# Performance work log

Measured on AMD Instinct MI355X. Metric: run time of the kernel, lower is better.

The kernel has to match this reference:

```python
import jax, jax.numpy as jnp
import numpy as np

N_POINTS = 2_000_000
N_BATCH = 8


def cart2polar(xyz):
    rho = jnp.sqrt(xyz[:, 0] ** 2 + xyz[:, 1] ** 2)
    phi = jnp.arctan2(xyz[:, 1], xyz[:, 0])
    return jnp.stack((rho, phi, xyz[:, 2]), axis=1)


def setup_inputs() -> dict:
    key = jax.random.key(0)
    k1, k2, k3, k4 = jax.random.split(key, 4)
    xy = jax.random.uniform(k1, (N_POINTS, 2), minval=-50.0, maxval=50.0)
    z = jax.random.uniform(k2, (N_POINTS, 1), minval=-4.0, maxval=2.0)
    inten = jax.random.uniform(k3, (N_POINTS, 1))
    points = jnp.concatenate([xy, z, inten], axis=1)  # [N, 4]
    batch_idx = jnp.sort(jax.random.randint(k4, (N_POINTS,), 0, N_BATCH)).astype(jnp.int32)
    coors_range_xyz = jnp.array([[0.0, 50.0], [-np.pi, np.pi], [-4.0, 2.0]], dtype=jnp.float32)
    spatial_shape = np.array([480, 360, 32])  # static
    scale_list = np.array([2, 4, 1])          # module appends 1; static
    return dict(points=points, batch_idx=batch_idx,
                coors_range_xyz=coors_range_xyz,
                spatial_shape=spatial_shape, scale_list=scale_list)


def _unique_rows(bxyz, dims):
    # Encode [b, gx, gy, gz] rows into a single int32 key (max 8*480*360*32 ~ 44M).
    key = ((bxyz[:, 0] * dims[0] + bxyz[:, 1]) * dims[1] + bxyz[:, 2]) * dims[2] + bxyz[:, 3]
    order = jnp.argsort(key)
    sk = key[order]
    flags = jnp.concatenate([jnp.ones((1,), bool), sk[1:] != sk[:-1]])
    rank = jnp.cumsum(flags.astype(jnp.int32)) - 1          # unique-id per sorted row
    inv = jnp.zeros_like(rank).at[order].set(rank)           # inverse map, like torch.unique
    # first occurrence of each unique row (all rows with same rank are identical)
    unq = jnp.zeros_like(bxyz).at[rank].set(bxyz[order])     # padded to [N, 4]
    num_unique = rank[-1] + 1
    return unq, inv, num_unique


def reference(points, batch_idx, coors_range_xyz, spatial_shape, scale_list):
    pc = points[:, :3]
    xyz_pol = cart2polar(pc)
    lo = coors_range_xyz[:, 0]
    hi = coors_range_xyz[:, 1]
    crop = hi - lo
    ss_np = np.asarray(spatial_shape)
    outs = []
    for scale in [int(s) for s in np.asarray(scale_list)]:
        cells = jnp.asarray(np.ceil(ss_np / scale) - 1.0, dtype=xyz_pol.dtype)
        grid = jnp.floor((jnp.clip(xyz_pol, lo, hi) - lo) / crop * cells).astype(jnp.int32)
        bxyz = jnp.concatenate([batch_idx[:, None].astype(jnp.int32), grid], axis=1)  # [N,4]
        dims = np.ceil(ss_np / scale).astype(np.int64)
        unq, inv, num = _unique_rows(bxyz, dims)
        # reorder unique coords as [b, z, y, x], cast int32 (torch: unq[:, [0,3,2,1]])
        coors = jnp.concatenate([unq[:, 0:1], unq[:, 3:4], unq[:, 2:3], unq[:, 1:2]], axis=1).astype(jnp.int32)
        outs.extend([bxyz, inv, coors, num])
    return tuple(outs)
```

## Files before the change

### kernel.cpp

```cpp
#include <hip/hip_runtime.h>
#include <cstdint>

#define DI __device__ __forceinline__

constexpr int NPTS       = 2000000;
constexpr int STRIDE_OUT = 18000001;
constexpr int OFF_INV    = 8000000;
constexpr int OFF_COORS  = 10000000;
constexpr int OFF_NUM    = 18000000;

constexpr int R2W  = 172800;
constexpr int R4W  = 21600;
constexpr int R1W  = 1382400;
constexpr int RW0  = 0;
constexpr int RW1  = R2W;
constexpr int RW2  = R2W + R4W;
constexpr int WTOT = R2W + R4W + R1W;
constexpr int NB1  = (WTOT + 1023) / 1024;
constexpr int J2   = 8;
constexpr int P1   = 6;
constexpr int J1   = 4;
constexpr int S1W  = 28800;
constexpr int S1BITS = S1W * 32;

constexpr int NBLK_INV   = (NPTS + 255) / 256;
constexpr int NBLK_INV8  = ((NBLK_INV + 7) / 8) * 8;
constexpr int INV_QUOT   = NBLK_INV8 / 8;
constexpr int NBLK_COORS = (WTOT + 255) / 256;
constexpr int NBLK_TAIL  = (3 * NPTS + 255) / 256;

DI float fmul_s(float a, float b){ float r; asm("v_mul_f32 %0, %1, %2" : "=v"(r) : "v"(a), "v"(b)); return r; }
DI float fadd_s(float a, float b){ float r; asm("v_add_f32 %0, %1, %2" : "=v"(r) : "v"(a), "v"(b)); return r; }

DI void compute_keys(float x, float y, float z, int b, int (&key)[3]) {
  const float PI_F     = 3.14159265358979323846f;
  const float TWO_PI_F = 6.28318530717958647692f;
  float rho = sqrtf(fadd_s(fmul_s(x, x), fmul_s(y, y)));
  float phi = atan2f(y, x);
  float tr = (fminf(fmaxf(rho, 0.0f), 50.0f) - 0.0f) / 50.0f;
  float tp = (fminf(fmaxf(phi, -PI_F), PI_F) + PI_F) / TWO_PI_F;
  float tz = (fminf(fmaxf(z, -4.0f), 2.0f) + 4.0f) / 6.0f;
  constexpr float C0[3] = {239.f, 119.f, 479.f};
  constexpr float C1[3] = {179.f,  89.f, 359.f};
  constexpr float C2[3] = { 15.f,   7.f,  31.f};
  constexpr int   D0[3] = {240, 120, 480};
  constexpr int   D1[3] = {180,  90, 360};
  constexpr int   D2[3] = { 16,   8,  32};
  #pragma unroll
  for (int s = 0; s < 3; ++s) {
    int a0 = (int)floorf(tr * C0[s]);
    int a1 = (int)floorf(tp * C1[s]);
    int a2 = (int)floorf(tz * C2[s]);
    key[s] = ((b * D0[s] + a0) * D1[s] + a1) * D2[s] + a2;
  }
}

__global__ __launch_bounds__(256) void pass_keys(const float4* __restrict__ pts,
                                                 const int* __restrict__ batch, int n,
                                                 int* __restrict__ keys,
                                                 int* __restrict__ bstart) {
  int i = blockIdx.x * 256 + threadIdx.x;
  if (i >= n) return;
  float4 p = pts[i];
  int bi = batch[i];
  int key[3];
  compute_keys(p.x, p.y, p.z, bi, key);
  keys[i] = key[0]; keys[n + i] = key[1]; keys[2 * n + i] = key[2];
  if (i == 0) {
    #pragma unroll 1
    for (int k = 0; k <= bi; ++k) bstart[k] = 0;
  }
  int bnext = (i + 1 < n) ? batch[i + 1] : 8;
  #pragma unroll 1
  for (int k = bi + 1; k <= bnext; ++k) bstart[k] = i + 1;
}

__global__ __launch_bounds__(1024) void hist_all(const int* __restrict__ bstart,
                                                 const int* __restrict__ keys, int n,
                                                 uint32_t* __restrict__ rep2s,
                                                 uint32_t* __restrict__ rep4s,
                                                 uint32_t* __restrict__ rep1s) {
  alignas(16) __shared__ uint32_t bmA[S1W];
  alignas(16) __shared__ uint32_t bmB[2700];
  int t = threadIdx.x;
  int pb = blockIdx.x;
  if (pb < 64) {
    int bv = pb & 7, j = pb >> 3;
    for (int w = t * 4; w < 21600; w += 4096) *reinterpret_cast<uint4*>(bmA + w) = make_uint4(0,0,0,0);
    for (int w = t; w < 2700; w += 1024) bmB[w] = 0;
    __syncthreads();
    int lo = bstart[bv];
    int hi = bstart[bv + 1];
    int sz = hi - lo;
    int s = lo + (int)((long long)sz * j / J2);
    int e = lo + (int)((long long)sz * (j + 1) / J2);
    const int* k0 = keys;
    const int* k1 = keys + n;
    for (int i = s + t; i < e; i += 1024) {
      int ink2 = k0[i] - bv * 691200;
      int ink4 = k1[i] - bv * 86400;
      atomicOr(&bmA[ink2 >> 5], 1u << (ink2 & 31));
      atomicOr(&bmB[ink4 >> 5], 1u << (ink4 & 31));
    }
    __syncthreads();
    uint32_t* d2 = rep2s + (size_t)j * R2W + bv * 21600;
    uint32_t* d4 = rep4s + (size_t)j * R4W + bv * 2700;
    for (int w = t * 4; w < 21600; w += 4096) *reinterpret_cast<uint4*>(d2 + w) = *reinterpret_cast<uint4*>(bmA + w);
    for (int w = t * 4; w < 2700; w += 4096) *reinterpret_cast<uint4*>(d4 + w) = *reinterpret_cast<uint4*>(bmB + w);
  } else {
    int bv = pb & 7;
    int id = (pb - 64) >> 3;
    int j = id / 6, r = id - j * 6;
    int slice = bv * 6 + r;
    for (int w = t * 4; w < S1W; w += 4096) *reinterpret_cast<uint4*>(bmA + w) = make_uint4(0,0,0,0);
    __syncthreads();
    int lo = bstart[bv];
    int hi = bstart[bv + 1];
    int sz = hi - lo;
    int s = lo + (int)((long long)sz * j / J1);
    int e = lo + (int)((long long)sz * (j + 1) / J1);
    const int* k2 = keys + 2 * n;
    int base = bv * 5529600 + r * S1BITS;
    for (int i = s + t; i < e; i += 1024) {
      int rel = k2[i] - base;
      if ((unsigned)rel < (unsigned)S1BITS) atomicOr(&bmA[rel >> 5], 1u << (rel & 31));
    }
    __syncthreads();
    uint32_t* d = rep1s + (size_t)j * R1W + (size_t)slice * S1W;
    for (int w = t * 4; w < S1W; w += 4096) *reinterpret_cast<uint4*>(d + w) = *reinterpret_cast<uint4*>(bmA + w);
  }
}

DI uint4 merged_words(int base, const uint32_t* __restrict__ rep2s,
                      const uint32_t* __restrict__ rep4s,
                      const uint32_t* __restrict__ rep1s) {
  uint4 acc = make_uint4(0, 0, 0, 0);
  if (base < RW1) {
    #pragma unroll
    for (int c = 0; c < J2; ++c) {
      uint4 w = *reinterpret_cast<const uint4*>(rep2s + (size_t)c * R2W + base);
      acc.x |= w.x; acc.y |= w.y; acc.z |= w.z; acc.w |= w.w;
    }
  } else if (base < RW2) {
    int l = base - RW1;
    #pragma unroll
    for (int c = 0; c < J2; ++c) {
      uint4 w = *reinterpret_cast<const uint4*>(rep4s + (size_t)c * R4W + l);
      acc.x |= w.x; acc.y |= w.y; acc.z |= w.z; acc.w |= w.w;
    }
  } else {
    int l = base - RW2;
    #pragma unroll
    for (int c = 0; c < J1; ++c) {
      uint4 w = *reinterpret_cast<const uint4*>(rep1s + (size_t)c * R1W + l);
      acc.x |= w.x; acc.y |= w.y; acc.z |= w.z; acc.w |= w.w;
    }
  }
  return acc;
}

__global__ __launch_bounds__(256) void scanA(const uint32_t* __restrict__ rep2s,
                                             const uint32_t* __restrict__ rep4s,
                                             const uint32_t* __restrict__ rep1s,
                                             uint32_t* __restrict__ bits,
                                             uint32_t* __restrict__ blockSums) {
  __shared__ uint32_t lds[256];
  int t = threadIdx.x;
  int base = blockIdx.x * 1024 + t * 4;
  uint32_t s = 0;
  if (base < WTOT) {
    uint4 m = merged_words(base, rep2s, rep4s, rep1s);
    *reinterpret_cast<uint4*>(bits + base) = m;
    s = __popc(m.x) + __popc(m.y) + __popc(m.z) + __popc(m.w);
  }
  lds[t] = s; __syncthreads();
  for (int off = 128; off > 0; off >>= 1) { if (t < off) lds[t] += lds[t + off]; __syncthreads(); }
  if (t == 0) blockSums[blockIdx.x] = lds[0];
}

__global__ __launch_bounds__(256) void scanC(const uint32_t* __restrict__ bits,
                                             const uint32_t* __restrict__ blockSums,
                                             uint2* __restrict__ pairs) {
  __shared__ uint32_t lds[256];
  int t = threadIdx.x;
  uint32_t bs = 0;
  for (int k = t; k < (int)blockIdx.x; k += 256) bs += blockSums[k];
  lds[t] = bs; __syncthreads();
  for (int off = 128; off > 0; off >>= 1) { if (t < off) lds[t] += lds[t + off]; __syncthreads(); }
  uint32_t blockBase = lds[0];
  __syncthreads();
  int base = blockIdx.x * 1024 + t * 4;
  uint32_t b[4] = {0,0,0,0}; uint32_t c[4]; uint32_t sum = 0;
  if (base < WTOT) {
    uint4 w = *reinterpret_cast<const uint4*>(bits + base);
    b[0] = w.x; b[1] = w.y; b[2] = w.z; b[3] = w.w;
  }
  #pragma unroll
  for (int k = 0; k < 4; ++k) { c[k] = __popc(b[k]); sum += c[k]; }
  lds[t] = sum; __syncthreads();
  for (int off = 1; off < 256; off <<= 1) {
    uint32_t x = (t >= off) ? lds[t - off] : 0u; __syncthreads();
    lds[t] += x; __syncthreads();
  }
  uint32_t excl = lds[t] - sum + blockBase;
  if (base < WTOT) {
    #pragma unroll
    for (int k = 0; k < 4; ++k) { pairs[base + k] = make_uint2(b[k], excl); excl += c[k]; }
  }
}

template <int S>
DI int4 decode_key(int key) {
  constexpr int D0[3] = {240, 120, 480};
  constexpr int D1[3] = {180,  90, 360};
  constexpr int D2[3] = { 16,   8,  32};
  int a2 = key & (D2[S] - 1);
  int r  = key / D2[S];
  int q  = r / D1[S];
  int a1 = r - q * D1[S];
  int b  = q / D0[S];
  int a0 = q - b * D0[S];
  return make_int4(b, a0, a1, a2);
}

template <int S>
DI void coors_word(int wi_local, uint32_t bits, uint32_t rank, int* __restrict__ coors) {
  int keybase = wi_local * 32;
  while (bits) {
    int j = __builtin_ctz(bits);
    bits &= bits - 1;
    int4 d = decode_key<S>(keybase + j);
    *reinterpret_cast<int4*>(coors + (size_t)rank * 4) = make_int4(d.x, d.w, d.z, d.y);
    ++rank;
  }
}

__global__ __launch_bounds__(256) void epilogue(int n, const uint2* __restrict__ pairs,
                                                const int* __restrict__ keys,
                                                int* __restrict__ out) {
  int b = blockIdx.x;
  int t = threadIdx.x;
  if (b < NBLK_INV8) {
    int l = (b & 7) * INV_QUOT + (b >> 3);
    if (l >= NBLK_INV) return;
    int i = l * 256 + t;
    if (i >= n) return;
    int key[3] = { keys[i], keys[n + i], keys[2 * n + i] };
    constexpr int RW[3] = {RW0, RW1, RW2};
    *reinterpret_cast<int4*>(out + 0 * STRIDE_OUT + i * 4) = decode_key<0>(key[0]);
    *reinterpret_cast<int4*>(out + 1 * STRIDE_OUT + i * 4) = decode_key<1>(key[1]);
    *reinterpret_cast<int4*>(out + 2 * STRIDE_OUT + i * 4) = decode_key<2>(key[2]);
    #pragma unroll
    for (int s = 0; s < 3; ++s) {
      uint2 pr = pairs[RW[s] + (key[s] >> 5)];
      uint32_t base = pr.y - ((s == 0) ? 0u : pairs[RW[s]].y);
      int rank = (int)(base + __popc(pr.x & ((1u << (key[s] & 31)) - 1u)));
      out[s * STRIDE_OUT + OFF_INV + i] = rank;
    }
  } else if (b < NBLK_INV8 + NBLK_COORS) {
    int wi = (b - NBLK_INV8) * 256 + t;
    if (wi >= WTOT) return;
    uint2 pr = pairs[wi];
    if (!pr.x) return;
    if (wi < RW1)      coors_word<0>(wi,       pr.x, pr.y,                 out + 0 * STRIDE_OUT + OFF_COORS);
    else if (wi < RW2) coors_word<1>(wi - RW1, pr.x, pr.y - pairs[RW1].y,  out + 1 * STRIDE_OUT + OFF_COORS);
    else               coors_word<2>(wi - RW2, pr.x, pr.y - pairs[RW2].y,  out + 2 * STRIDE_OUT + OFF_COORS);
  } else {
    int idx = (b - NBLK_INV8 - NBLK_COORS) * 256 + t;
    if (idx >= 3 * n) return;
    int s = 0, i = idx;
    if (i >= 2 * n)  { s = 2; i -= 2 * n; }
    else if (i >= n) { s = 1; i -= n; }
    uint2 last = pairs[WTOT - 1];
    uint32_t total = last.y + (uint32_t)__popc(last.x);
    uint32_t lo = (s == 0) ? 0u : pairs[(s == 1) ? RW1 : RW2].y;
    uint32_t hi = (s == 0) ? pairs[RW1].y : (s == 1) ? pairs[RW2].y : total;
    uint32_t num = hi - lo;
    if (i == 0) out[s * STRIDE_OUT + OFF_NUM] = (int)num;
    if ((uint32_t)i >= num)
      *reinterpret_cast<int4*>(out + s * STRIDE_OUT + OFF_COORS + (size_t)i * 4) = make_int4(0, 0, 0, 0);
  }
}

extern "C" void kernel_launch(void* const* d_in, const int* in_sizes, int n_in,
                              void* d_out, int out_size, void* d_ws, size_t ws_size,
                              hipStream_t stream) {
  const float4* pts   = (const float4*)d_in[0];
  const int*    batch = (const int*)d_in[1];
  int n = in_sizes[1];
  int* out = (int*)d_out;

  uint32_t* rep2s     = (uint32_t*)d_ws;
  uint32_t* rep4s     = rep2s + (size_t)J2 * R2W;
  uint32_t* rep1s     = rep4s + (size_t)J2 * R4W;
  uint32_t* bits      = rep1s + (size_t)J1 * R1W;
  uint2*    pairs     = (uint2*)(bits + WTOT);
  uint32_t* blockSums = (uint32_t*)(pairs + WTOT);
  int*      bstart    = (int*)(blockSums + NB1);
  int*      keys      = (int*)(bstart + 16);

  int nblk = (n + 255) / 256;
  pass_keys<<<nblk, 256, 0, stream>>>(pts, batch, n, keys, bstart);
  hist_all<<<256, 1024, 0, stream>>>(bstart, keys, n, rep2s, rep4s, rep1s);
  scanA<<<NB1, 256, 0, stream>>>(rep2s, rep4s, rep1s, bits, blockSums);
  scanC<<<NB1, 256, 0, stream>>>(bits, blockSums, pairs);
  epilogue<<<NBLK_INV8 + NBLK_COORS + NBLK_TAIL, 256, 0, stream>>>(n, pairs, keys, out);
}
```

Measured before the change: 328.2 us.

## Pre-bucket scale-1 keys by radial slice so histogram reads only its slice

The key pass now scatters each scale-1 key into a per-(batch, radial-slice) bucket buffer, using block-local shared counters and one global atomic per bucket. The scale-1 histogram blocks then read only their own bucket instead of scanning every key in the batch and discarding the out-of-slice ones, which cuts redundant global reads by roughly the slice count. Scale-2 and scale-4 keys are packed into an int2 array so each is fetched with one load. The cost is extra scatter writes and atomics in the key pass, a memset, fixed bucket capacities that assume an even spread of points, and reuse of the bits buffer as bucket storage.

```diff
diff --git a/kernel.cpp b/kernel.cpp
--- a/kernel.cpp
+++ b/kernel.cpp
@@ -18,10 +18,13 @@
 constexpr int WTOT = R2W + R4W + R1W;
 constexpr int NB1  = (WTOT + 1023) / 1024;
 constexpr int J2   = 8;
-constexpr int P1   = 6;
 constexpr int J1   = 4;
 constexpr int S1W  = 28800;
 constexpr int S1BITS = S1W * 32;
+
+constexpr int BCAP[6]  = {12288, 24576, 36864, 49152, 61440, 126976};
+constexpr int BOFF[6]  = {0, 12288, 36864, 73728, 122880, 184320};
+constexpr int BSTRIDE  = 311296;
 
 constexpr int NBLK_INV   = (NPTS + 255) / 256;
 constexpr int NBLK_INV8  = ((NBLK_INV + 7) / 8) * 8;
@@ -32,51 +35,72 @@
 DI float fmul_s(float a, float b){ float r; asm("v_mul_f32 %0, %1, %2" : "=v"(r) : "v"(a), "v"(b)); return r; }
 DI float fadd_s(float a, float b){ float r; asm("v_add_f32 %0, %1, %2" : "=v"(r) : "v"(a), "v"(b)); return r; }
 
-DI void compute_keys(float x, float y, float z, int b, int (&key)[3]) {
-  const float PI_F     = 3.14159265358979323846f;
-  const float TWO_PI_F = 6.28318530717958647692f;
-  float rho = sqrtf(fadd_s(fmul_s(x, x), fmul_s(y, y)));
-  float phi = atan2f(y, x);
-  float tr = (fminf(fmaxf(rho, 0.0f), 50.0f) - 0.0f) / 50.0f;
-  float tp = (fminf(fmaxf(phi, -PI_F), PI_F) + PI_F) / TWO_PI_F;
-  float tz = (fminf(fmaxf(z, -4.0f), 2.0f) + 4.0f) / 6.0f;
-  constexpr float C0[3] = {239.f, 119.f, 479.f};
-  constexpr float C1[3] = {179.f,  89.f, 359.f};
-  constexpr float C2[3] = { 15.f,   7.f,  31.f};
-  constexpr int   D0[3] = {240, 120, 480};
-  constexpr int   D1[3] = {180,  90, 360};
-  constexpr int   D2[3] = { 16,   8,  32};
-  #pragma unroll
-  for (int s = 0; s < 3; ++s) {
-    int a0 = (int)floorf(tr * C0[s]);
-    int a1 = (int)floorf(tp * C1[s]);
-    int a2 = (int)floorf(tz * C2[s]);
-    key[s] = ((b * D0[s] + a0) * D1[s] + a1) * D2[s] + a2;
-  }
-}
-
 __global__ __launch_bounds__(256) void pass_keys(const float4* __restrict__ pts,
                                                  const int* __restrict__ batch, int n,
-                                                 int* __restrict__ keys,
-                                                 int* __restrict__ bstart) {
-  int i = blockIdx.x * 256 + threadIdx.x;
-  if (i >= n) return;
-  float4 p = pts[i];
-  int bi = batch[i];
-  int key[3];
-  compute_keys(p.x, p.y, p.z, bi, key);
-  keys[i] = key[0]; keys[n + i] = key[1]; keys[2 * n + i] = key[2];
-  if (i == 0) {
+                                                 int2* __restrict__ keys01,
+                                                 int* __restrict__ keys2,
+                                                 int* __restrict__ bstart,
+                                                 int* __restrict__ bucketCnt,
+                                                 uint32_t* __restrict__ bucketBuf) {
+  __shared__ int cnt[48], gbase[48];
+  int t = threadIdx.x;
+  int i = blockIdx.x * 256 + t;
+  bool act = (i < n);
+  if (t < 48) cnt[t] = 0;
+  __syncthreads();
+
+  int k[3] = {0, 0, 0};
+  int bi = 0, bk = 0, slot = 0;
+  if (act) {
+    float4 p = pts[i];
+    bi = batch[i];
+    const float PI_F     = 3.14159265358979323846f;
+    const float TWO_PI_F = 6.28318530717958647692f;
+    float rho = sqrtf(fadd_s(fmul_s(p.x, p.x), fmul_s(p.y, p.y)));
+    float phi = atan2f(p.y, p.x);
+    float tr = (fminf(fmaxf(rho, 0.0f), 50.0f) - 0.0f) / 50.0f;
+    float tp = (fminf(fmaxf(phi, -PI_F), PI_F) + PI_F) / TWO_PI_F;
+    float tz = (fminf(fmaxf(p.z, -4.0f), 2.0f) + 4.0f) / 6.0f;
+    constexpr float C0[3] = {239.f, 119.f, 479.f};
+    constexpr float C1[3] = {179.f,  89.f, 359.f};
+    constexpr float C2[3] = { 15.f,   7.f,  31.f};
+    constexpr int   D0[3] = {240, 120, 480};
+    constexpr int   D1[3] = {180,  90, 360};
+    constexpr int   D2[3] = { 16,   8,  32};
+    int a0f = 0;
+    #pragma unroll
+    for (int s = 0; s < 3; ++s) {
+      int a0 = (int)floorf(tr * C0[s]);
+      int a1 = (int)floorf(tp * C1[s]);
+      int a2 = (int)floorf(tz * C2[s]);
+      k[s] = ((bi * D0[s] + a0) * D1[s] + a1) * D2[s] + a2;
+      if (s == 2) a0f = a0;
+    }
+    bk = bi * 6 + a0f / 80;
+    slot = atomicAdd(&cnt[bk], 1);
+  }
+  __syncthreads();
+  if (t < 48) gbase[t] = cnt[t] ? atomicAdd(&bucketCnt[t], cnt[t]) : 0;
+  __syncthreads();
+  if (act) {
+    keys01[i] = make_int2(k[0], k[1]);
+    keys2[i]  = k[2];
+    int bv = bk / 6, r = bk - bv * 6;
+    bucketBuf[(size_t)bv * BSTRIDE + BOFF[r] + gbase[bk] + slot] = (uint32_t)k[2];
+    if (i == 0) {
+      #pragma unroll 1
+      for (int kk = 0; kk <= bi; ++kk) bstart[kk] = 0;
+    }
+    int bnext = (i + 1 < n) ? batch[i + 1] : 8;
     #pragma unroll 1
-    for (int k = 0; k <= bi; ++k) bstart[k] = 0;
-  }
-  int bnext = (i + 1 < n) ? batch[i + 1] : 8;
-  #pragma unroll 1
-  for (int k = bi + 1; k <= bnext; ++k) bstart[k] = i + 1;
+    for (int kk = bi + 1; kk <= bnext; ++kk) bstart[kk] = i + 1;
+  }
 }
 
 __global__ __launch_bounds__(1024) void hist_all(const int* __restrict__ bstart,
-                                                 const int* __restrict__ keys, int n,
+                                                 const int2* __restrict__ keys01,
+                                                 const int* __restrict__ bucketCnt,
+                                                 const uint32_t* __restrict__ bucketBuf, int n,
                                                  uint32_t* __restrict__ rep2s,
                                                  uint32_t* __restrict__ rep4s,
                                                  uint32_t* __restrict__ rep1s) {
@@ -94,11 +118,12 @@
     int sz = hi - lo;
     int s = lo + (int)((long long)sz * j / J2);
     int e = lo + (int)((long long)sz * (j + 1) / J2);
-    const int* k0 = keys;
-    const int* k1 = keys + n;
+    int b2 = bv * 691200;
+    int b4 = bv * 86400;
     for (int i = s + t; i < e; i += 1024) {
-      int ink2 = k0[i] - bv * 691200;
-      int ink4 = k1[i] - bv * 86400;
+      int2 kk = keys01[i];
+      int ink2 = kk.x - b2;
+      int ink4 = kk.y - b4;
       atomicOr(&bmA[ink2 >> 5], 1u << (ink2 & 31));
       atomicOr(&bmB[ink4 >> 5], 1u << (ink4 & 31));
     }
@@ -114,16 +139,14 @@
     int slice = bv * 6 + r;
     for (int w = t * 4; w < S1W; w += 4096) *reinterpret_cast<uint4*>(bmA + w) = make_uint4(0,0,0,0);
     __syncthreads();
-    int lo = bstart[bv];
-    int hi = bstart[bv + 1];
-    int sz = hi - lo;
-    int s = lo + (int)((long long)sz * j / J1);
-    int e = lo + (int)((long long)sz * (j + 1) / J1);
-    const int* k2 = keys + 2 * n;
-    int base = bv * 5529600 + r * S1BITS;
+    int c = bucketCnt[slice];
+    int s = (int)((long long)c * j / J1);
+    int e = (int)((long long)c * (j + 1) / J1);
+    const uint32_t* src = bucketBuf + (size_t)bv * BSTRIDE + BOFF[r];
+    int sub = bv * 5529600 + r * S1BITS;
     for (int i = s + t; i < e; i += 1024) {
-      int rel = k2[i] - base;
-      if ((unsigned)rel < (unsigned)S1BITS) atomicOr(&bmA[rel >> 5], 1u << (rel & 31));
+      int rel = (int)src[i] - sub;
+      atomicOr(&bmA[rel >> 5], 1u << (rel & 31));
     }
     __syncthreads();
     uint32_t* d = rep1s + (size_t)j * R1W + (size_t)slice * S1W;
@@ -236,7 +259,8 @@
 }
 
 __global__ __launch_bounds__(256) void epilogue(int n, const uint2* __restrict__ pairs,
-                                                const int* __restrict__ keys,
+                                                const int2* __restrict__ keys01,
+                                                const int* __restrict__ keys2,
                                                 int* __restrict__ out) {
   int b = blockIdx.x;
   int t = threadIdx.x;
@@ -245,11 +269,12 @@
     if (l >= NBLK_INV) return;
     int i = l * 256 + t;
     if (i >= n) return;
-    int key[3] = { keys[i], keys[n + i], keys[2 * n + i] };
+    int2 k01 = keys01[i];
+    int key[3] = { k01.x, k01.y, keys2[i] };
     constexpr int RW[3] = {RW0, RW1, RW2};
-    *reinterpret_cast<int4*>(out + 0 * STRIDE_OUT + i * 4) = decode_key<0>(key[0]);
-    *reinterpret_cast<int4*>(out + 1 * STRIDE_OUT + i * 4) = decode_key<1>(key[1]);
-    *reinterpret_cast<int4*>(out + 2 * STRIDE_OUT + i * 4) = decode_key<2>(key[2]);
+    *reinterpret_cast<int4*>(out + 0 * STRIDE_OUT + (size_t)i * 4) = decode_key<0>(key[0]);
+    *reinterpret_cast<int4*>(out + 1 * STRIDE_OUT + (size_t)i * 4) = decode_key<1>(key[1]);
+    *reinterpret_cast<int4*>(out + 2 * STRIDE_OUT + (size_t)i * 4) = decode_key<2>(key[2]);
     #pragma unroll
     for (int s = 0; s < 3; ++s) {
       uint2 pr = pairs[RW[s] + (key[s] >> 5)];
@@ -296,13 +321,17 @@
   uint32_t* bits      = rep1s + (size_t)J1 * R1W;
   uint2*    pairs     = (uint2*)(bits + WTOT);
   uint32_t* blockSums = (uint32_t*)(pairs + WTOT);
-  int*      bstart    = (int*)(blockSums + NB1);
-  int*      keys      = (int*)(bstart + 16);
-
+  int*      bstart    = (int*)(blockSums + 1544);
+  int*      bucketCnt = bstart + 16;
+  int2*     keys01    = (int2*)(bucketCnt + 48);
+  int*      keys2     = (int*)(keys01 + NPTS);
+  uint32_t* bucketBuf = bits;
+
+  hipMemsetAsync(bucketCnt, 0, 48 * sizeof(int), stream);
   int nblk = (n + 255) / 256;
-  pass_keys<<<nblk, 256, 0, stream>>>(pts, batch, n, keys, bstart);
-  hist_all<<<256, 1024, 0, stream>>>(bstart, keys, n, rep2s, rep4s, rep1s);
+  pass_keys<<<nblk, 256, 0, stream>>>(pts, batch, n, keys01, keys2, bstart, bucketCnt, bucketBuf);
+  hist_all<<<256, 1024, 0, stream>>>(bstart, keys01, bucketCnt, bucketBuf, n, rep2s, rep4s, rep1s);
   scanA<<<NB1, 256, 0, stream>>>(rep2s, rep4s, rep1s, bits, blockSums);
   scanC<<<NB1, 256, 0, stream>>>(bits, blockSums, pairs);
-  epilogue<<<NBLK_INV8 + NBLK_COORS + NBLK_TAIL, 256, 0, stream>>>(n, pairs, keys, out);
-}
+  epilogue<<<NBLK_INV8 + NBLK_COORS + NBLK_TAIL, 256, 0, stream>>>(n, pairs, keys01, keys2, out);
+}
```

Measured after the change: 386.4 us. 17.7% more time.
